# Optimization experiments

Hardware: AMD Instinct MI355X
Metric: run time of the kernel (lower is better)

## Reference

```python
import jax, jax.numpy as jnp
import numpy as np

# Static configuration matching the selected code path:
#   mode='inject_subject', is_self_attn=True, layer_id='up_blocks.0' (inject layer, bank hit)
#   alpha = AlphaScheduler.alpha(step=20, total=50, 'up_blocks.0') = 0.8 * 0.6 = 0.48
B, L, D, H = 4, 1024, 1280, 20
DH = D // H  # 64
ALPHA = 0.48


def setup_inputs() -> dict:
    key = jax.random.key(0)
    ks = jax.random.split(key, 8)
    w = lambda k, shp: (jax.random.normal(k, shp, dtype=jnp.float32) * 0.02)
    return {
        "hidden_states": jax.random.normal(ks[0], (B, L, D), dtype=jnp.float32),
        "Wq": w(ks[1], (D, D)),
        "Wk": w(ks[2], (D, D)),
        "Wv": w(ks[3], (D, D)),
        "Wo": w(ks[4], (D, D)),
        "bo": jnp.zeros((D,), dtype=jnp.float32),
        # cached background K/V, stored after head_to_batch_dim -> [B*H, L_bg, DH]
        "K_bg": jax.random.normal(ks[5], (B * H, L, DH), dtype=jnp.float32),
        "V_bg": jax.random.normal(ks[6], (B * H, L, DH), dtype=jnp.float32),
    }


def _head_to_batch(x):  # [B, L, D] -> [B*H, L, DH]
    b, l, _ = x.shape
    return x.reshape(b, l, H, DH).transpose(0, 2, 1, 3).reshape(b * H, l, DH)


def _batch_to_head(x):  # [B*H, L, DH] -> [B, L, D]
    bh, l, _ = x.shape
    b = bh // H
    return x.reshape(b, H, l, DH).transpose(0, 2, 1, 3).reshape(b, l, D)


def reference(hidden_states, Wq, Wk, Wv, Wo, bo, K_bg, V_bg):
    # q/k/v projections (self-attention: k, v from hidden_states)
    q = _head_to_batch(hidden_states @ Wq)  # [B*H, L, DH]
    k = _head_to_batch(hidden_states @ Wk)
    v = _head_to_batch(hidden_states @ Wv)

    # inject_subject: concat cached background K/V scaled by alpha along kv-seq dim
    k = jnp.concatenate([k, ALPHA * K_bg], axis=1)  # [B*H, 2L, DH]
    v = jnp.concatenate([v, ALPHA * V_bg], axis=1)

    # _sdpa: q scaled by scale*sqrt(dh), SDPA divides by sqrt(dh) -> net factor `scale`
    scale = 1.0 / jnp.sqrt(jnp.asarray(DH, dtype=q.dtype))
    scores = jnp.einsum('bqd,bkd->bqk', q, k) * scale  # [B*H, L, 2L]
    probs = jax.nn.softmax(scores, axis=-1)
    context = jnp.einsum('bqk,bkd->bqd', probs, v)  # [B*H, L, DH]

    out = _batch_to_head(context) @ Wo + bo  # to_out[0] linear
    return out
```

## Files before the change

kernel.cpp:

```cpp
#include <hip/hip_runtime.h>
#include <hip/hip_bf16.h>

#define B_   4
#define L_   1024
#define D_   1280
#define H_   20
#define DH_  64
#define BH_  (B_*H_)
#define L2_  (2*L_)
#define ALPHA_ 0.48f
#define QSCALE_ 0.180336880f

typedef __attribute__((ext_vector_type(8))) short short8;
typedef __attribute__((ext_vector_type(4))) float float4v;

__device__ __forceinline__ float exp2_fast(float x) {
    float r;
    asm volatile("v_exp_f32 %0, %1" : "=v"(r) : "v"(x));
    return r;
}

__device__ __forceinline__ ushort f2bf(float f) {
    union { float f; unsigned int i; } v; v.f = f;
    unsigned int i = v.i;
    unsigned int r = i + 0x7FFF + ((i >> 16) & 1);
    return (ushort)(r >> 16);
}
__device__ __forceinline__ short8 pack8(float4 f0, float4 f1) {
    short8 o;
    o[0] = (short)f2bf(f0.x); o[1] = (short)f2bf(f0.y);
    o[2] = (short)f2bf(f0.z); o[3] = (short)f2bf(f0.w);
    o[4] = (short)f2bf(f1.x); o[5] = (short)f2bf(f1.y);
    o[6] = (short)f2bf(f1.z); o[7] = (short)f2bf(f1.w);
    return o;
}
__device__ __forceinline__ void pack4_store(ushort* dst, float a, float b, float c, float d) {
    union { __hip_bfloat162 h; unsigned int u; } x, y;
    x.h = __float22bfloat162_rn(make_float2(a, b));
    y.h = __float22bfloat162_rn(make_float2(c, d));
    uint2 v; v.x = x.u; v.y = y.u;
    *(uint2*)dst = v;
}

__device__ __forceinline__ void async16(const void* g, void* l) {
    __builtin_amdgcn_global_load_lds(
        (__attribute__((address_space(1))) void*)g,
        (__attribute__((address_space(3))) void*)l, 16, 0, 0);
}

__global__ __launch_bounds__(256) void prep(
    const float* __restrict__ w0, const float* __restrict__ w1,
    const float* __restrict__ w2, const float* __restrict__ w3,
    ushort* __restrict__ Wt,
    const float* __restrict__ Vbg, ushort* __restrict__ Vt,
    const float* __restrict__ X, ushort* __restrict__ Xb,
    const float* __restrict__ Kbg, ushort* __restrict__ Kcv) {
    int bi = blockIdx.x, tid = threadIdx.x;
    if (bi < 2880) {
        bool doScale = (bi >= 1600);
        const float* src; ushort* dst; int srcld, dstld; long sbase, dbase;
        if (bi < 1600) {
            int z = bi / 400, t4 = bi % 400;
            int by = t4 / 20, bx = t4 % 20;
            const float* srcs[4] = {w0, w1, w2, w3};
            src = srcs[z]; srcld = D_; dstld = D_;
            sbase = (long)(by * 64) * D_ + bx * 64;
            dst = Wt + (long)z * D_ * D_;
            dbase = (long)(bx * 64) * D_ + by * 64;
        } else {
            int j = bi - 1600;
            int bh = j >> 4, kt = j & 15;
            src = Vbg; srcld = DH_; dstld = L2_;
            sbase = ((long)bh * L_ + kt * 64) * DH_;
            dst = Vt;
            dbase = (long)bh * DH_ * L2_ + L_ + kt * 64;
        }
        __shared__ ushort t[64 * 72];
        int ldr = tid >> 3, ldc = (tid & 7) * 8;
#pragma unroll
        for (int i = 0; i < 2; i++) {
            int y = ldr + 32 * i;
            long idx = sbase + (long)y * srcld + ldc;
            float4 f0 = *(const float4*)&src[idx];
            float4 f1 = *(const float4*)&src[idx + 4];
            if (doScale) {
                f0.x *= ALPHA_; f0.y *= ALPHA_; f0.z *= ALPHA_; f0.w *= ALPHA_;
                f1.x *= ALPHA_; f1.y *= ALPHA_; f1.z *= ALPHA_; f1.w *= ALPHA_;
            }
            *(short8*)&t[y * 72 + ldc] = pack8(f0, f1);
        }
        __syncthreads();
        int r8 = (tid & 7) * 8, c0 = tid >> 3;
#pragma unroll
        for (int i = 0; i < 2; i++) {
            int c = c0 + i * 32;
            short8 o;
#pragma unroll
            for (int j2 = 0; j2 < 8; j2++) o[j2] = (short)t[(r8 + j2) * 72 + c];
            *(short8*)&dst[dbase + (long)c * dstld + r8] = o;
        }
    } else if (bi < 5440) {
        long i = ((long)(bi - 2880) * 256 + tid) * 8;
        *(short8*)&Xb[i] = pack8(*(const float4*)&X[i], *(const float4*)&X[i + 4]);
    } else {
        long i = ((long)(bi - 5440) * 256 + tid) * 8;
        *(short8*)&Kcv[i] = pack8(*(const float4*)&Kbg[i], *(const float4*)&Kbg[i + 4]);
    }
}

template<int BMt, int BNt, int WROWS, int WCOLS>
__global__ __launch_bounds__(256) void gemm_tpl(
    const ushort* __restrict__ A, const ushort* __restrict__ Bt,
    ushort* __restrict__ Qp, ushort* __restrict__ Kp, ushort* __restrict__ Vt,
    float* __restrict__ Out, const float* __restrict__ bo, int mode) {
    constexpr int MI = BMt / WROWS / 16;
    constexpr int NI = BNt / WCOLS / 16;
    constexpr int ASZ = BMt * 32, BSZ = BNt * 32;
    constexpr int RB = 1280 / BNt;
    __shared__ __align__(16) ushort Al[2 * ASZ];
    __shared__ __align__(16) ushort Bl[2 * BSZ];
    int tid = threadIdx.x;
    int bx = blockIdx.x, by = blockIdx.y;
    int w = tid >> 6, lane = tid & 63, l15 = lane & 15, quad = lane >> 4;
    int wm = (w / WCOLS) * (BMt / WROWS);
    int wn = (w % WCOLS) * (BNt / WCOLS);
    float4v acc[MI][NI] = {};
    const int K = 1280;
    constexpr int NK = 40;
    const ushort* Arow = A + (long)by * BMt * K + (tid >> 2) * K + (tid & 3) * 8;
    const ushort* Brow = Bt + (long)bx * BNt * K + (tid >> 2) * K + (tid & 3) * 8;

    auto stage = [&](int ki, int b) {
#pragma unroll
        for (int i = 0; i < BMt / 64; i++)
            async16(Arow + (long)i * 64 * K + ki * 32, &Al[b * ASZ + (i * 4 + w) * 512]);
#pragma unroll
        for (int i = 0; i < BNt / 64; i++)
            async16(Brow + (long)i * 64 * K + ki * 32, &Bl[b * BSZ + (i * 4 + w) * 512]);
    };

    stage(0, 0);
    __syncthreads();
    for (int ki = 0; ki < NK; ki++) {
        int cur = ki & 1;
        if (ki + 1 < NK) stage(ki + 1, 1 - cur);
        short8 av[MI], bv[NI];
#pragma unroll
        for (int mi = 0; mi < MI; mi++)
            av[mi] = *(const short8*)&Al[cur * ASZ + (wm + mi * 16 + l15) * 32 + quad * 8];
#pragma unroll
        for (int ni = 0; ni < NI; ni++)
            bv[ni] = *(const short8*)&Bl[cur * BSZ + (wn + ni * 16 + l15) * 32 + quad * 8];
#pragma unroll
        for (int mi = 0; mi < MI; mi++)
#pragma unroll
            for (int ni = 0; ni < NI; ni++)
                acc[mi][ni] = __builtin_amdgcn_mfma_f32_16x16x32_bf16(av[mi], bv[ni], acc[mi][ni], 0, 0, 0);
        __syncthreads();
    }

    if (mode == 0) {
        int which = bx / RB;
#pragma unroll
        for (int mi = 0; mi < MI; mi++) {
            int m0 = by * BMt + wm + mi * 16 + quad * 4;
            int b = m0 >> 10, l0 = m0 & 1023;
#pragma unroll
            for (int ni = 0; ni < NI; ni++) {
                int n = bx * BNt + wn + ni * 16 + l15;
                int np = n - which * 1280;
                int h = np >> 6, dh = np & 63;
                if (which == 0) {
#pragma unroll
                    for (int r = 0; r < 4; r++)
                        Qp[((long)(b * H_ + h) * L_ + l0 + r) * DH_ + dh] =
                            f2bf(acc[mi][ni][r] * QSCALE_);
                } else if (which == 1) {
#pragma unroll
                    for (int r = 0; r < 4; r++)
                        Kp[((long)(b * H_ + h) * L_ + l0 + r) * DH_ + dh] =
                            f2bf(acc[mi][ni][r]);
                } else {
                    pack4_store(&Vt[((long)(b * H_ + h) * DH_ + dh) * L2_ + l0],
                                acc[mi][ni][0], acc[mi][ni][1],
                                acc[mi][ni][2], acc[mi][ni][3]);
                }
            }
        }
    } else {
#pragma unroll
        for (int mi = 0; mi < MI; mi++) {
            int mloc = wm + mi * 16 + quad * 4;
#pragma unroll
            for (int ni = 0; ni < NI; ni++) {
                int nloc = wn + ni * 16 + l15;
#pragma unroll
                for (int r = 0; r < 4; r++) {
                    int m = by * BMt + mloc + r;
                    int n = bx * BNt + nloc;
                    Out[(long)m * D_ + n] = acc[mi][ni][r] + bo[n];
                }
            }
        }
    }
}

#define FS 72

__global__ __launch_bounds__(512) void flash_attn(
    const ushort* __restrict__ Qp, const ushort* __restrict__ Kp,
    const ushort* __restrict__ Kbg, const ushort* __restrict__ Vt,
    ushort* __restrict__ Ctx) {
    __shared__ __align__(16) ushort Kl[2 * 4096], Vl[2 * 4096];
    __shared__ __align__(16) ushort Pl[128 * FS];
    int tid = threadIdx.x;
    int w = tid >> 6, lane = tid & 63, l15 = lane & 15, quad = lane >> 4;
    int bi = blockIdx.x;
    int bh = (bi & 7) * 10 + ((bi >> 3) % 10);
    int qt = bi / 80;

    short8 aq[2];
    const ushort* Qb = Qp + ((long)bh * L_ + qt * 128 + w * 16) * DH_;
#pragma unroll
    for (int ks = 0; ks < 2; ks++)
        aq[ks] = *(const short8*)&Qb[l15 * DH_ + ks * 32 + quad * 8];

    float rs = 0.f;
    float4v O[4] = {};
    const ushort* Vb = Vt + (long)bh * DH_ * L2_;
    int prow = (w * 16 + l15) * FS;

    auto stage = [&](int kt, int b) {
        const ushort* Ksrc = (kt < 16)
            ? Kp  + ((long)bh * L_ + kt * 64) * DH_
            : Kbg + ((long)bh * L_ + (kt - 16) * 64) * DH_;
        async16(&Ksrc[(long)lane * DH_ + w * 8], &Kl[b * 4096 + w * 512]);
        async16(&Vb[(long)lane * L2_ + kt * 64 + w * 8], &Vl[b * 4096 + w * 512]);
    };

    stage(0, 0);
    __syncthreads();
    for (int kt = 0; kt < 32; kt++) {
        int cur = kt & 1;
        if (kt + 1 < 32) stage(kt + 1, 1 - cur);
        bool bg = (kt >= 16);
        short8 bk[2][4];
#pragma unroll
        for (int ks = 0; ks < 2; ks++)
#pragma unroll
            for (int nt = 0; nt < 4; nt++)
                bk[ks][nt] = *(const short8*)&Kl[cur * 4096 + (ks * 4 + quad) * 512 + (nt * 16 + l15) * 8];
        float4v s[4] = {};
#pragma unroll
        for (int ks = 0; ks < 2; ks++)
#pragma unroll
            for (int nt = 0; nt < 4; nt++)
                s[nt] = __builtin_amdgcn_mfma_f32_16x16x32_bf16(bk[ks][nt], aq[ks], s[nt], 0, 0, 0);
#pragma unroll
        for (int nt = 0; nt < 4; nt++) {
            float p[4];
#pragma unroll
            for (int r = 0; r < 4; r++) {
                float sv = s[nt][r];
                if (bg) sv *= ALPHA_;
                p[r] = exp2_fast(sv);
                rs += p[r];
            }
            pack4_store(&Pl[prow + nt * 16 + quad * 4], p[0], p[1], p[2], p[3]);
        }
        short8 bv[2][4];
#pragma unroll
        for (int ks = 0; ks < 2; ks++)
#pragma unroll
            for (int nt = 0; nt < 4; nt++)
                bv[ks][nt] = *(const short8*)&Vl[cur * 4096 + (ks * 4 + quad) * 512 + (nt * 16 + l15) * 8];
        asm volatile("s_waitcnt lgkmcnt(0)" ::: "memory");
#pragma unroll
        for (int ks = 0; ks < 2; ks++) {
            short8 ap = *(const short8*)&Pl[prow + ks * 32 + quad * 8];
#pragma unroll
            for (int nt = 0; nt < 4; nt++)
                O[nt] = __builtin_amdgcn_mfma_f32_16x16x32_bf16(bv[ks][nt], ap, O[nt], 0, 0, 0);
        }
        __syncthreads();
    }
    float v = rs;
    v += __shfl_xor(v, 16);
    v += __shfl_xor(v, 32);
    float rcp = 1.f / v;
    int b = bh / H_, h = bh % H_;
    long l = qt * 128 + w * 16 + l15;
#pragma unroll
    for (int nt = 0; nt < 4; nt++)
        pack4_store(&Ctx[(long)(b * L_ + l) * D_ + h * DH_ + nt * 16 + quad * 4],
                    O[nt][0] * rcp, O[nt][1] * rcp, O[nt][2] * rcp, O[nt][3] * rcp);
}

extern "C" void kernel_launch(void* const* d_in, const int* in_sizes, int n_in,
                              void* d_out, int out_size, void* d_ws, size_t ws_size,
                              hipStream_t stream) {
    const float* X   = (const float*)d_in[0];
    const float* Wq  = (const float*)d_in[1];
    const float* Wk  = (const float*)d_in[2];
    const float* Wv  = (const float*)d_in[3];
    const float* Wo  = (const float*)d_in[4];
    const float* bo  = (const float*)d_in[5];
    const float* Kbg = (const float*)d_in[6];
    const float* Vbg = (const float*)d_in[7];

    char* ws = (char*)d_ws;
    size_t off = 0;
    auto alloc = [&](size_t bytes) {
        void* p = ws + off;
        off = (off + bytes + 255) & ~(size_t)255;
        return p;
    };
    ushort* Wt    = (ushort*)alloc((size_t)4 * D_ * D_ * 2);
    ushort* Qp    = (ushort*)alloc((size_t)BH_ * L_ * DH_ * 2);
    ushort* Kp    = (ushort*)alloc((size_t)BH_ * L_ * DH_ * 2);
    ushort* Kcv   = (ushort*)alloc((size_t)BH_ * L_ * DH_ * 2);
    ushort* Vt    = (ushort*)alloc((size_t)BH_ * DH_ * L2_ * 2);
    ushort* Xb    = (ushort*)alloc((size_t)B_ * L_ * D_ * 2);
    ushort* Ctx   = Xb;
    ushort* Wqkv_t = Wt;
    ushort* Wo_t   = Wt + (size_t)3 * D_ * D_;

    prep<<<8000, 256, 0, stream>>>(Wq, Wk, Wv, Wo, Wt, Vbg, Vt, X, Xb, Kbg, Kcv);
    gemm_tpl<128, 128, 2, 2><<<dim3(30, 32), 256, 0, stream>>>(
        Xb, Wqkv_t, Qp, Kp, Vt, nullptr, nullptr, 0);
    flash_attn<<<dim3(640), 512, 0, stream>>>(Qp, Kp, Kcv, Vt, Ctx);
    gemm_tpl<64, 128, 1, 4><<<dim3(10, 64), 256, 0, stream>>>(
        Ctx, Wo_t, nullptr, nullptr, nullptr, (float*)d_out, bo, 1);
}
```

Measured before the change: 315.7 us.

## Use 4 waves per attention block, each computing 32 query rows

Flash attention now runs 256 threads per block, with each wave handling two 16-row query tiles instead of one. Every K/V fragment read from LDS feeds twice as many MFMAs, which cuts LDS read traffic per FLOP, and each thread issues two async copies per stage. A sched_barrier is placed after the LDS wait so that P and V loads are not reordered across it. The cost is more registers per thread (two sets of accumulators and scores) and fewer waves per block, which may reduce latency hiding.

```diff
diff --git a/kernel.cpp b/kernel.cpp
--- a/kernel.cpp
+++ b/kernel.cpp
@@ -207,7 +207,7 @@
 
 #define FS 72
 
-__global__ __launch_bounds__(512) void flash_attn(
+__global__ __launch_bounds__(256) void flash_attn(
     const ushort* __restrict__ Qp, const ushort* __restrict__ Kp,
     const ushort* __restrict__ Kbg, const ushort* __restrict__ Vt,
     ushort* __restrict__ Ctx) {
@@ -219,23 +219,29 @@
     int bh = (bi & 7) * 10 + ((bi >> 3) % 10);
     int qt = bi / 80;
 
-    short8 aq[2];
-    const ushort* Qb = Qp + ((long)bh * L_ + qt * 128 + w * 16) * DH_;
-#pragma unroll
-    for (int ks = 0; ks < 2; ks++)
-        aq[ks] = *(const short8*)&Qb[l15 * DH_ + ks * 32 + quad * 8];
-
-    float rs = 0.f;
-    float4v O[4] = {};
+    short8 aq[2][2];
+    const ushort* Qb = Qp + ((long)bh * L_ + qt * 128 + w * 32) * DH_;
+#pragma unroll
+    for (int mi = 0; mi < 2; mi++)
+#pragma unroll
+        for (int ks = 0; ks < 2; ks++)
+            aq[mi][ks] = *(const short8*)&Qb[(mi * 16 + l15) * DH_ + ks * 32 + quad * 8];
+
+    float rs[2] = {0.f, 0.f};
+    float4v O[2][4] = {};
     const ushort* Vb = Vt + (long)bh * DH_ * L2_;
-    int prow = (w * 16 + l15) * FS;
+    int prow = (w * 32 + l15) * FS;
 
     auto stage = [&](int kt, int b) {
         const ushort* Ksrc = (kt < 16)
             ? Kp  + ((long)bh * L_ + kt * 64) * DH_
             : Kbg + ((long)bh * L_ + (kt - 16) * 64) * DH_;
-        async16(&Ksrc[(long)lane * DH_ + w * 8], &Kl[b * 4096 + w * 512]);
-        async16(&Vb[(long)lane * L2_ + kt * 64 + w * 8], &Vl[b * 4096 + w * 512]);
+#pragma unroll
+        for (int i = 0; i < 2; i++) {
+            int c = w * 2 + i;
+            async16(&Ksrc[(long)lane * DH_ + c * 8], &Kl[b * 4096 + c * 512]);
+            async16(&Vb[(long)lane * L2_ + kt * 64 + c * 8], &Vl[b * 4096 + c * 512]);
+        }
     };
 
     stage(0, 0);
@@ -244,56 +250,68 @@
         int cur = kt & 1;
         if (kt + 1 < 32) stage(kt + 1, 1 - cur);
         bool bg = (kt >= 16);
-        short8 bk[2][4];
-#pragma unroll
-        for (int ks = 0; ks < 2; ks++)
+        float4v s[4][2] = {};
+#pragma unroll
+        for (int ks = 0; ks < 2; ks++) {
+            short8 bk[4];
 #pragma unroll
             for (int nt = 0; nt < 4; nt++)
-                bk[ks][nt] = *(const short8*)&Kl[cur * 4096 + (ks * 4 + quad) * 512 + (nt * 16 + l15) * 8];
-        float4v s[4] = {};
-#pragma unroll
-        for (int ks = 0; ks < 2; ks++)
+                bk[nt] = *(const short8*)&Kl[cur * 4096 + (ks * 4 + quad) * 512 + (nt * 16 + l15) * 8];
 #pragma unroll
             for (int nt = 0; nt < 4; nt++)
-                s[nt] = __builtin_amdgcn_mfma_f32_16x16x32_bf16(bk[ks][nt], aq[ks], s[nt], 0, 0, 0);
-#pragma unroll
-        for (int nt = 0; nt < 4; nt++) {
-            float p[4];
-#pragma unroll
-            for (int r = 0; r < 4; r++) {
-                float sv = s[nt][r];
-                if (bg) sv *= ALPHA_;
-                p[r] = exp2_fast(sv);
-                rs += p[r];
+#pragma unroll
+                for (int mi = 0; mi < 2; mi++)
+                    s[nt][mi] = __builtin_amdgcn_mfma_f32_16x16x32_bf16(bk[nt], aq[mi][ks], s[nt][mi], 0, 0, 0);
+        }
+#pragma unroll
+        for (int nt = 0; nt < 4; nt++)
+#pragma unroll
+            for (int mi = 0; mi < 2; mi++) {
+                float p[4];
+#pragma unroll
+                for (int r = 0; r < 4; r++) {
+                    float sv = s[nt][mi][r];
+                    if (bg) sv *= ALPHA_;
+                    p[r] = exp2_fast(sv);
+                    rs[mi] += p[r];
+                }
+                pack4_store(&Pl[prow + mi * 16 * FS + nt * 16 + quad * 4],
+                            p[0], p[1], p[2], p[3]);
             }
-            pack4_store(&Pl[prow + nt * 16 + quad * 4], p[0], p[1], p[2], p[3]);
-        }
-        short8 bv[2][4];
-#pragma unroll
-        for (int ks = 0; ks < 2; ks++)
+        asm volatile("s_waitcnt lgkmcnt(0)" ::: "memory");
+        __builtin_amdgcn_sched_barrier(0);
+#pragma unroll
+        for (int ks = 0; ks < 2; ks++) {
+            short8 bv[4];
 #pragma unroll
             for (int nt = 0; nt < 4; nt++)
-                bv[ks][nt] = *(const short8*)&Vl[cur * 4096 + (ks * 4 + quad) * 512 + (nt * 16 + l15) * 8];
-        asm volatile("s_waitcnt lgkmcnt(0)" ::: "memory");
-#pragma unroll
-        for (int ks = 0; ks < 2; ks++) {
-            short8 ap = *(const short8*)&Pl[prow + ks * 32 + quad * 8];
+                bv[nt] = *(const short8*)&Vl[cur * 4096 + (ks * 4 + quad) * 512 + (nt * 16 + l15) * 8];
+            short8 ap[2];
+#pragma unroll
+            for (int mi = 0; mi < 2; mi++)
+                ap[mi] = *(const short8*)&Pl[prow + mi * 16 * FS + ks * 32 + quad * 8];
 #pragma unroll
             for (int nt = 0; nt < 4; nt++)
-                O[nt] = __builtin_amdgcn_mfma_f32_16x16x32_bf16(bv[ks][nt], ap, O[nt], 0, 0, 0);
+#pragma unroll
+                for (int mi = 0; mi < 2; mi++)
+                    O[mi][nt] = __builtin_amdgcn_mfma_f32_16x16x32_bf16(bv[nt], ap[mi], O[mi][nt], 0, 0, 0);
         }
         __syncthreads();
     }
-    float v = rs;
-    v += __shfl_xor(v, 16);
-    v += __shfl_xor(v, 32);
-    float rcp = 1.f / v;
     int b = bh / H_, h = bh % H_;
-    long l = qt * 128 + w * 16 + l15;
-#pragma unroll
-    for (int nt = 0; nt < 4; nt++)
-        pack4_store(&Ctx[(long)(b * L_ + l) * D_ + h * DH_ + nt * 16 + quad * 4],
-                    O[nt][0] * rcp, O[nt][1] * rcp, O[nt][2] * rcp, O[nt][3] * rcp);
+#pragma unroll
+    for (int mi = 0; mi < 2; mi++) {
+        float v = rs[mi];
+        v += __shfl_xor(v, 16);
+        v += __shfl_xor(v, 32);
+        float rcp = 1.f / v;
+        long l = qt * 128 + w * 32 + mi * 16 + l15;
+#pragma unroll
+        for (int nt = 0; nt < 4; nt++)
+            pack4_store(&Ctx[(long)(b * L_ + l) * D_ + h * DH_ + nt * 16 + quad * 4],
+                        O[mi][nt][0] * rcp, O[mi][nt][1] * rcp,
+                        O[mi][nt][2] * rcp, O[mi][nt][3] * rcp);
+    }
 }
 
 extern "C" void kernel_launch(void* const* d_in, const int* in_sizes, int n_in,
@@ -328,7 +346,7 @@
     prep<<<8000, 256, 0, stream>>>(Wq, Wk, Wv, Wo, Wt, Vbg, Vt, X, Xb, Kbg, Kcv);
     gemm_tpl<128, 128, 2, 2><<<dim3(30, 32), 256, 0, stream>>>(
         Xb, Wqkv_t, Qp, Kp, Vt, nullptr, nullptr, 0);
-    flash_attn<<<dim3(640), 512, 0, stream>>>(Qp, Kp, Kcv, Vt, Ctx);
+    flash_attn<<<dim3(640), 256, 0, stream>>>(Qp, Kp, Kcv, Vt, Ctx);
     gemm_tpl<64, 128, 1, 4><<<dim3(10, 64), 256, 0, stream>>>(
         Ctx, Wo_t, nullptr, nullptr, nullptr, (float*)d_out, bo, 1);
 }
```

Result: no change. 311.8 us (-1.2%).
